# Performance work log

Measured on AMD Instinct MI355X. Metric: run time of the kernel, lower is better.

The kernel has to match this reference:

```python
import jax, jax.numpy as jnp
import numpy as np

# EfficientMemoryGEMMWithSoftmax forward: the returned value visible to the
# model is simply result = x1 @ x2 (batched GEMM of softmax probs with V).
# The outlier-statistics / sparse / SVD compression path only affects what is
# cached for the (lossy) backward; the forward output math is exact.

B, H, S, D = 2, 16, 2048, 64

def setup_inputs() -> dict:
    key = jax.random.key(0)
    k1, k2 = jax.random.split(key)
    # x1 ~ softmax probabilities: nonnegative, rows normalized over last axis
    logits = jax.random.normal(k1, (B, H, S, S), dtype=jnp.float32)
    x1 = jax.nn.softmax(logits, axis=-1)
    x2 = jax.random.normal(k2, (B, H, S, D), dtype=jnp.float32)
    return {"x1": x1, "x2": x2}

def reference(x1, x2):
    # [B,H,S,S] @ [B,H,S,D] -> [B,H,S,D]
    return jnp.einsum('bhsk,bhkd->bhsd', x1, x2)
```

## Files before the change

### kernel.cpp

```cpp
#include <hip/hip_runtime.h>
#include <hip/hip_bf16.h>


#define S_DIM 2048
#define D_DIM 64
#define BM 128
#define BK 128
#define NT (S_DIM / BK)
#define LDB (BK + 8)

typedef __attribute__((ext_vector_type(8))) short short8;
typedef __attribute__((ext_vector_type(4))) short short4v;
typedef __attribute__((ext_vector_type(4))) float f32x4;

__device__ __forceinline__ short f2bf(float x) {
    return __builtin_bit_cast(short, __float2bfloat16(x));
}

__global__ __launch_bounds__(512, 2)
void pv_gemm_kernel(const float* __restrict__ x1,
                    const float* __restrict__ x2,
                    float* __restrict__ out) {
    __shared__ short lds_b[2][D_DIM][LDB];

    int bid = blockIdx.x;
    int lb  = (bid & 7) * 64 + (bid >> 3);
    int bh   = lb >> 4;
    int mblk = lb & 15;
    int m0   = mblk * BM;

    int tid  = threadIdx.x;
    int lane = tid & 63;
    int w    = tid >> 6;

    int sd  = tid & 63;
    int skb = tid >> 6;
    const float* x2base = x2 + (size_t)bh * S_DIM * D_DIM + sd;

    int arow = m0 + w * 16 + (lane & 15);
    int kgrp = (lane >> 4) * 8;
    const float* abase = x1 + ((size_t)bh * S_DIM + arow) * S_DIM + kgrp;

    f32x4 acc[4];
#pragma unroll
    for (int i = 0; i < 4; ++i) acc[i] = (f32x4){0.f, 0.f, 0.f, 0.f};

    {
        float rs[16];
#pragma unroll
        for (int i = 0; i < 16; ++i)
            rs[i] = x2base[(size_t)(skb * 16 + i) * D_DIM];
#pragma unroll
        for (int j = 0; j < 4; ++j) {
            short4v v;
            v[0] = f2bf(rs[4 * j + 0]);
            v[1] = f2bf(rs[4 * j + 1]);
            v[2] = f2bf(rs[4 * j + 2]);
            v[3] = f2bf(rs[4 * j + 3]);
            *(short4v*)&lds_b[0][sd][skb * 16 + 4 * j] = v;
        }
    }

    int buf = 0;
    for (int t = 0; t < NT; ++t) {
        __syncthreads();

        float rn[16];
        if (t + 1 < NT) {
            const float* p = x2base + (size_t)(t + 1) * BK * D_DIM;
#pragma unroll
            for (int i = 0; i < 16; ++i)
                rn[i] = p[(size_t)(skb * 16 + i) * D_DIM];
        }

        const float* ab = abase + (size_t)t * BK;
#pragma unroll
        for (int kk = 0; kk < 4; ++kk) {
            float4 lo = *(const float4*)(ab + kk * 32);
            float4 hi = *(const float4*)(ab + kk * 32 + 4);
            short8 a;
            a[0] = f2bf(lo.x); a[1] = f2bf(lo.y); a[2] = f2bf(lo.z); a[3] = f2bf(lo.w);
            a[4] = f2bf(hi.x); a[5] = f2bf(hi.y); a[6] = f2bf(hi.z); a[7] = f2bf(hi.w);
#pragma unroll
            for (int ni = 0; ni < 4; ++ni) {
                int col = ni * 16 + (lane & 15);
                const short8* bp =
                    (const short8*)&lds_b[buf][col][kk * 32 + kgrp];
                acc[ni] = __builtin_amdgcn_mfma_f32_16x16x32_bf16(a, *bp, acc[ni], 0, 0, 0);
            }
        }

        if (t + 1 < NT) {
#pragma unroll
            for (int j = 0; j < 4; ++j) {
                short4v v;
                v[0] = f2bf(rn[4 * j + 0]);
                v[1] = f2bf(rn[4 * j + 1]);
                v[2] = f2bf(rn[4 * j + 2]);
                v[3] = f2bf(rn[4 * j + 3]);
                *(short4v*)&lds_b[buf ^ 1][sd][skb * 16 + 4 * j] = v;
            }
        }
        buf ^= 1;
    }

    int col0 = lane & 15;
    int r0   = m0 + w * 16 + ((lane >> 4) << 2);
    float* ob = out + ((size_t)bh * S_DIM + r0) * D_DIM + col0;
#pragma unroll
    for (int ni = 0; ni < 4; ++ni) {
#pragma unroll
        for (int r = 0; r < 4; ++r)
            ob[(size_t)r * D_DIM + ni * 16] = acc[ni][r];
    }
}

extern "C" void kernel_launch(void* const* d_in, const int* in_sizes, int n_in,
                              void* d_out, int out_size, void* d_ws, size_t ws_size,
                              hipStream_t stream) {
    const float* x1 = (const float*)d_in[0];
    const float* x2 = (const float*)d_in[1];
    float* out = (float*)d_out;

    dim3 grid(512);
    dim3 block(512);
    hipLaunchKernelGGL(pv_gemm_kernel, grid, block, 0, stream, x1, x2, out);
}
```

Before: 132.0 us.

## Prefetch A tiles into registers one step ahead and raise occupancy target

Loads the next K-tile of the fp32 probability matrix into a second register buffer while the current tile is converted and fed to MFMA. The loop is manually unrolled by two to alternate buffers. The launch bound is raised to request four blocks per CU. The aim is to hide global-load latency on the dominant x1 stream, at the cost of more live registers and a possible spill under the tighter register cap.

```diff
diff --git a/kernel.cpp b/kernel.cpp
--- a/kernel.cpp
+++ b/kernel.cpp
@@ -17,7 +17,7 @@
     return __builtin_bit_cast(short, __float2bfloat16(x));
 }
 
-__global__ __launch_bounds__(512, 2)
+__global__ __launch_bounds__(512, 4)
 void pv_gemm_kernel(const float* __restrict__ x1,
                     const float* __restrict__ x2,
                     float* __restrict__ out) {
@@ -61,48 +61,67 @@
         }
     }
 
-    int buf = 0;
-    for (int t = 0; t < NT; ++t) {
-        __syncthreads();
+    float4 rA0[8], rA1[8];
+#pragma unroll
+    for (int kk = 0; kk < 4; ++kk) {
+        rA0[2 * kk]     = *(const float4*)(abase + kk * 32);
+        rA0[2 * kk + 1] = *(const float4*)(abase + kk * 32 + 4);
+    }
 
-        float rn[16];
-        if (t + 1 < NT) {
-            const float* p = x2base + (size_t)(t + 1) * BK * D_DIM;
-#pragma unroll
-            for (int i = 0; i < 16; ++i)
-                rn[i] = p[(size_t)(skb * 16 + i) * D_DIM];
-        }
+#define ITER(T, RBUF, RA_CUR, RA_NXT)                                        \
+    {                                                                        \
+        __syncthreads();                                                     \
+        float rn[16];                                                        \
+        if ((T) + 1 < NT) {                                                  \
+                      \
+            const float* p = x2base + (size_t)((T) + 1) * BK * D_DIM;        \
+            _Pragma("unroll")                                                \
+            for (int i = 0; i < 16; ++i)                                     \
+                rn[i] = p[(size_t)(skb * 16 + i) * D_DIM];                   \
+            const float* an = abase + (size_t)((T) + 1) * BK;                \
+            _Pragma("unroll")                                                \
+            for (int kk = 0; kk < 4; ++kk) {                                 \
+                RA_NXT[2 * kk]     = *(const float4*)(an + kk * 32);         \
+                RA_NXT[2 * kk + 1] = *(const float4*)(an + kk * 32 + 4);     \
+            }                                                                \
+        }                                                                    \
+        _Pragma("unroll")                                                    \
+        for (int kk = 0; kk < 4; ++kk) {                                     \
+            short8 a;                                                        \
+            a[0] = f2bf(RA_CUR[2 * kk].x);                                   \
+            a[1] = f2bf(RA_CUR[2 * kk].y);                                   \
+            a[2] = f2bf(RA_CUR[2 * kk].z);                                   \
+            a[3] = f2bf(RA_CUR[2 * kk].w);                                   \
+            a[4] = f2bf(RA_CUR[2 * kk + 1].x);                               \
+            a[5] = f2bf(RA_CUR[2 * kk + 1].y);                               \
+            a[6] = f2bf(RA_CUR[2 * kk + 1].z);                               \
+            a[7] = f2bf(RA_CUR[2 * kk + 1].w);                               \
+            _Pragma("unroll")                                                \
+            for (int ni = 0; ni < 4; ++ni) {                                 \
+                const short8* bp = (const short8*)                           \
+                    &lds_b[RBUF][ni * 16 + (lane & 15)][kk * 32 + kgrp];     \
+                acc[ni] = __builtin_amdgcn_mfma_f32_16x16x32_bf16(           \
+                    a, *bp, acc[ni], 0, 0, 0);                               \
+            }                                                                \
+        }                                                                    \
+        if ((T) + 1 < NT) {                                                  \
+            _Pragma("unroll")                                                \
+            for (int j = 0; j < 4; ++j) {                                    \
+                short4v v;                                                   \
+                v[0] = f2bf(rn[4 * j + 0]);                                  \
+                v[1] = f2bf(rn[4 * j + 1]);                                  \
+                v[2] = f2bf(rn[4 * j + 2]);                                  \
+                v[3] = f2bf(rn[4 * j + 3]);                                  \
+                *(short4v*)&lds_b[(RBUF) ^ 1][sd][skb * 16 + 4 * j] = v;     \
+            }                                                                \
+        }                                                                    \
+    }
 
-        const float* ab = abase + (size_t)t * BK;
-#pragma unroll
-        for (int kk = 0; kk < 4; ++kk) {
-            float4 lo = *(const float4*)(ab + kk * 32);
-            float4 hi = *(const float4*)(ab + kk * 32 + 4);
-            short8 a;
-            a[0] = f2bf(lo.x); a[1] = f2bf(lo.y); a[2] = f2bf(lo.z); a[3] = f2bf(lo.w);
-            a[4] = f2bf(hi.x); a[5] = f2bf(hi.y); a[6] = f2bf(hi.z); a[7] = f2bf(hi.w);
-#pragma unroll
-            for (int ni = 0; ni < 4; ++ni) {
-                int col = ni * 16 + (lane & 15);
-                const short8* bp =
-                    (const short8*)&lds_b[buf][col][kk * 32 + kgrp];
-                acc[ni] = __builtin_amdgcn_mfma_f32_16x16x32_bf16(a, *bp, acc[ni], 0, 0, 0);
-            }
-        }
-
-        if (t + 1 < NT) {
-#pragma unroll
-            for (int j = 0; j < 4; ++j) {
-                short4v v;
-                v[0] = f2bf(rn[4 * j + 0]);
-                v[1] = f2bf(rn[4 * j + 1]);
-                v[2] = f2bf(rn[4 * j + 2]);
-                v[3] = f2bf(rn[4 * j + 3]);
-                *(short4v*)&lds_b[buf ^ 1][sd][skb * 16 + 4 * j] = v;
-            }
-        }
-        buf ^= 1;
+    for (int t = 0; t < NT; t += 2) {
+        ITER(t,     0, rA0, rA1);
+        ITER(t + 1, 1, rA1, rA0);
     }
+#undef ITER
 
     int col0 = lane & 15;
     int r0   = m0 + w * 16 + ((lane >> 4) << 2);
```

Result: faster. 116.8 us (-11.5%).

## Pre-transpose V to bf16 and read B operand directly from L2

Applied to the files above, without the earlier changes.

Adds a small pre-pass that converts x2 to bf16 and transposes it into workspace. The main GEMM then loads B fragments straight from global memory (L2-resident) instead of staging them through LDS, which removes the __syncthreads and LDS traffic. It also double-buffers the x1 loads in registers using nontemporal loads, and keeps the LDS kernel as a fallback when the workspace is too small. The cost is an extra kernel launch, extra register pressure, and more L2 traffic for B.

```diff
diff --git a/kernel.cpp b/kernel.cpp
--- a/kernel.cpp
+++ b/kernel.cpp
@@ -17,12 +17,36 @@
     return __builtin_bit_cast(short, __float2bfloat16(x));
 }
 
+__global__ __launch_bounds__(256)
+void x2_transpose_kernel(const float* __restrict__ x2, short* __restrict__ x2t) {
+    __shared__ float tile[64][65];
+    int bh = blockIdx.x >> 5;
+    int kb = (blockIdx.x & 31) * 64;
+    int t  = threadIdx.x;
+    int d  = t & 63;
+    int k4 = t >> 6;
+    const float* src = x2 + ((size_t)bh * S_DIM + kb) * D_DIM + d;
+#pragma unroll
+    for (int i = 0; i < 16; ++i)
+        tile[i * 4 + k4][d] = src[(size_t)(i * 4 + k4) * D_DIM];
+    __syncthreads();
+    int dcol = t >> 2;
+    int kg   = (t & 3) * 16;
+    short8 v0, v1;
+#pragma unroll
+    for (int j = 0; j < 8; ++j) {
+        v0[j] = f2bf(tile[kg + j][dcol]);
+        v1[j] = f2bf(tile[kg + 8 + j][dcol]);
+    }
+    short* dst = x2t + ((size_t)bh * D_DIM + dcol) * S_DIM + kb + kg;
+    *(short8*)dst = v0;
+    *(short8*)(dst + 8) = v1;
+}
+
 __global__ __launch_bounds__(512, 2)
-void pv_gemm_kernel(const float* __restrict__ x1,
-                    const float* __restrict__ x2,
-                    float* __restrict__ out) {
-    __shared__ short lds_b[2][D_DIM][LDB];
-
+void pv_gemm_l2b_kernel(const float* __restrict__ x1,
+                        const short* __restrict__ x2t,
+                        float* __restrict__ out) {
     int bid = blockIdx.x;
     int lb  = (bid & 7) * 64 + (bid >> 3);
     int bh   = lb >> 4;
@@ -33,18 +57,112 @@
     int lane = tid & 63;
     int w    = tid >> 6;
 
+    int arow = m0 + w * 16 + (lane & 15);
+    int kgrp = (lane >> 4) * 8;
+    const float* aptr = x1 + ((size_t)bh * S_DIM + arow) * S_DIM + kgrp;
+
+    const short* bbase = x2t + ((size_t)bh * D_DIM + (lane & 15)) * S_DIM + kgrp;
+    const short* bp_ni0 = bbase;
+    const short* bp_ni1 = bbase + (size_t)16 * S_DIM;
+    const short* bp_ni2 = bbase + (size_t)32 * S_DIM;
+    const short* bp_ni3 = bbase + (size_t)48 * S_DIM;
+
+    f32x4 acc[4];
+#pragma unroll
+    for (int i = 0; i < 4; ++i) acc[i] = (f32x4){0.f, 0.f, 0.f, 0.f};
+
+    f32x4 rA0[8], rA1[8];
+#pragma unroll
+    for (int kk = 0; kk < 4; ++kk) {
+        rA0[2 * kk]     = __builtin_nontemporal_load((const f32x4*)(aptr + kk * 32));
+        rA0[2 * kk + 1] = __builtin_nontemporal_load((const f32x4*)(aptr + kk * 32 + 4));
+    }
+
+#define ITER(T, RA_CUR, RA_NXT)                                               \
+    {                                                                         \
+        const short* b0 = bp_ni0 + (size_t)(T) * BK;                          \
+        const short* b1 = bp_ni1 + (size_t)(T) * BK;                          \
+        const short* b2 = bp_ni2 + (size_t)(T) * BK;                          \
+        const short* b3 = bp_ni3 + (size_t)(T) * BK;                          \
+        short8 vb[16];                                                        \
+        _Pragma("unroll")                                                     \
+        for (int kk = 0; kk < 4; ++kk) {                                      \
+            vb[kk * 4 + 0] = *(const short8*)(b0 + kk * 32);                  \
+            vb[kk * 4 + 1] = *(const short8*)(b1 + kk * 32);                  \
+            vb[kk * 4 + 2] = *(const short8*)(b2 + kk * 32);                  \
+            vb[kk * 4 + 3] = *(const short8*)(b3 + kk * 32);                  \
+        }                                                                     \
+        if ((T) + 1 < NT) {                                                   \
+            const float* an = aptr + (size_t)((T) + 1) * BK;                  \
+            _Pragma("unroll")                                                 \
+            for (int kk = 0; kk < 4; ++kk) {                                  \
+                RA_NXT[2 * kk] = __builtin_nontemporal_load(                  \
+                    (const f32x4*)(an + kk * 32));                            \
+                RA_NXT[2 * kk + 1] = __builtin_nontemporal_load(              \
+                    (const f32x4*)(an + kk * 32 + 4));                        \
+            }                                                                 \
+        }                                                                     \
+        _Pragma("unroll")                                                     \
+        for (int kk = 0; kk < 4; ++kk) {                                      \
+            short8 a;                                                         \
+            a[0] = f2bf(RA_CUR[2 * kk][0]);                                   \
+            a[1] = f2bf(RA_CUR[2 * kk][1]);                                   \
+            a[2] = f2bf(RA_CUR[2 * kk][2]);                                   \
+            a[3] = f2bf(RA_CUR[2 * kk][3]);                                   \
+            a[4] = f2bf(RA_CUR[2 * kk + 1][0]);                               \
+            a[5] = f2bf(RA_CUR[2 * kk + 1][1]);                               \
+            a[6] = f2bf(RA_CUR[2 * kk + 1][2]);                               \
+            a[7] = f2bf(RA_CUR[2 * kk + 1][3]);                               \
+            acc[0] = __builtin_amdgcn_mfma_f32_16x16x32_bf16(                 \
+                a, vb[kk * 4 + 0], acc[0], 0, 0, 0);                          \
+            acc[1] = __builtin_amdgcn_mfma_f32_16x16x32_bf16(                 \
+                a, vb[kk * 4 + 1], acc[1], 0, 0, 0);                          \
+            acc[2] = __builtin_amdgcn_mfma_f32_16x16x32_bf16(                 \
+                a, vb[kk * 4 + 2], acc[2], 0, 0, 0);                          \
+            acc[3] = __builtin_amdgcn_mfma_f32_16x16x32_bf16(                 \
+                a, vb[kk * 4 + 3], acc[3], 0, 0, 0);                          \
+        }                                                                     \
+    }
+
+    for (int t = 0; t < NT; t += 2) {
+        ITER(t,     rA0, rA1);
+        ITER(t + 1, rA1, rA0);
+    }
+#undef ITER
+
+    int col0 = lane & 15;
+    int r0   = m0 + w * 16 + ((lane >> 4) << 2);
+    float* ob = out + ((size_t)bh * S_DIM + r0) * D_DIM + col0;
+#pragma unroll
+    for (int ni = 0; ni < 4; ++ni) {
+#pragma unroll
+        for (int r = 0; r < 4; ++r)
+            ob[(size_t)r * D_DIM + ni * 16] = acc[ni][r];
+    }
+}
+
+__global__ __launch_bounds__(512, 4)
+void pv_gemm_lds_kernel(const float* __restrict__ x1,
+                        const float* __restrict__ x2,
+                        float* __restrict__ out) {
+    __shared__ short lds_b[2][D_DIM][LDB];
+    int bid = blockIdx.x;
+    int lb  = (bid & 7) * 64 + (bid >> 3);
+    int bh   = lb >> 4;
+    int mblk = lb & 15;
+    int m0   = mblk * BM;
+    int tid  = threadIdx.x;
+    int lane = tid & 63;
+    int w    = tid >> 6;
     int sd  = tid & 63;
     int skb = tid >> 6;
     const float* x2base = x2 + (size_t)bh * S_DIM * D_DIM + sd;
-
     int arow = m0 + w * 16 + (lane & 15);
     int kgrp = (lane >> 4) * 8;
     const float* abase = x1 + ((size_t)bh * S_DIM + arow) * S_DIM + kgrp;
-
     f32x4 acc[4];
 #pragma unroll
     for (int i = 0; i < 4; ++i) acc[i] = (f32x4){0.f, 0.f, 0.f, 0.f};
-
     {
         float rs[16];
 #pragma unroll
@@ -53,18 +171,14 @@
 #pragma unroll
         for (int j = 0; j < 4; ++j) {
             short4v v;
-            v[0] = f2bf(rs[4 * j + 0]);
-            v[1] = f2bf(rs[4 * j + 1]);
-            v[2] = f2bf(rs[4 * j + 2]);
-            v[3] = f2bf(rs[4 * j + 3]);
+            v[0] = f2bf(rs[4 * j + 0]); v[1] = f2bf(rs[4 * j + 1]);
+            v[2] = f2bf(rs[4 * j + 2]); v[3] = f2bf(rs[4 * j + 3]);
             *(short4v*)&lds_b[0][sd][skb * 16 + 4 * j] = v;
         }
     }
-
     int buf = 0;
     for (int t = 0; t < NT; ++t) {
         __syncthreads();
-
         float rn[16];
         if (t + 1 < NT) {
             const float* p = x2base + (size_t)(t + 1) * BK * D_DIM;
@@ -72,7 +186,6 @@
             for (int i = 0; i < 16; ++i)
                 rn[i] = p[(size_t)(skb * 16 + i) * D_DIM];
         }
-
         const float* ab = abase + (size_t)t * BK;
 #pragma unroll
         for (int kk = 0; kk < 4; ++kk) {
@@ -83,27 +196,22 @@
             a[4] = f2bf(hi.x); a[5] = f2bf(hi.y); a[6] = f2bf(hi.z); a[7] = f2bf(hi.w);
 #pragma unroll
             for (int ni = 0; ni < 4; ++ni) {
-                int col = ni * 16 + (lane & 15);
                 const short8* bp =
-                    (const short8*)&lds_b[buf][col][kk * 32 + kgrp];
+                    (const short8*)&lds_b[buf][ni * 16 + (lane & 15)][kk * 32 + kgrp];
                 acc[ni] = __builtin_amdgcn_mfma_f32_16x16x32_bf16(a, *bp, acc[ni], 0, 0, 0);
             }
         }
-
         if (t + 1 < NT) {
 #pragma unroll
             for (int j = 0; j < 4; ++j) {
                 short4v v;
-                v[0] = f2bf(rn[4 * j + 0]);
-                v[1] = f2bf(rn[4 * j + 1]);
-                v[2] = f2bf(rn[4 * j + 2]);
-                v[3] = f2bf(rn[4 * j + 3]);
+                v[0] = f2bf(rn[4 * j + 0]); v[1] = f2bf(rn[4 * j + 1]);
+                v[2] = f2bf(rn[4 * j + 2]); v[3] = f2bf(rn[4 * j + 3]);
                 *(short4v*)&lds_b[buf ^ 1][sd][skb * 16 + 4 * j] = v;
             }
         }
         buf ^= 1;
     }
-
     int col0 = lane & 15;
     int r0   = m0 + w * 16 + ((lane >> 4) << 2);
     float* ob = out + ((size_t)bh * S_DIM + r0) * D_DIM + col0;
@@ -122,7 +230,15 @@
     const float* x2 = (const float*)d_in[1];
     float* out = (float*)d_out;
 
-    dim3 grid(512);
-    dim3 block(512);
-    hipLaunchKernelGGL(pv_gemm_kernel, grid, block, 0, stream, x1, x2, out);
-}
+    const size_t need = (size_t)32 * D_DIM * S_DIM * sizeof(short);
+    if (ws_size >= need) {
+        short* x2t = (short*)d_ws;
+        hipLaunchKernelGGL(x2_transpose_kernel, dim3(1024), dim3(256), 0, stream,
+                           x2, x2t);
+        hipLaunchKernelGGL(pv_gemm_l2b_kernel, dim3(512), dim3(512), 0, stream,
+                           x1, x2t, out);
+    } else {
+        hipLaunchKernelGGL(pv_gemm_lds_kernel, dim3(512), dim3(512), 0, stream,
+                           x1, x2, out);
+    }
+}
```

Result: slower. 235.2 us (+78.2%).

## Split K in halves with whole-half B staged in LDS and atomic reduction

Applied to the files above, without the earlier changes.

Each block now covers a 256-row M tile and half of K. The whole 1024x64 bf16 slice of x2 is loaded into swizzled LDS once, which removes the per-step barriers and the double-buffered B. A-tile loads are register double-buffered, and each wave starts at a staggered K phase to spread DRAM and L2 traffic. Partial results are combined with float atomics into a zero-initialised output (an added memset), which costs extra atomic traffic and makes the summation order nondeterministic.

```diff
diff --git a/kernel.cpp b/kernel.cpp
--- a/kernel.cpp
+++ b/kernel.cpp
@@ -4,13 +4,12 @@
 
 #define S_DIM 2048
 #define D_DIM 64
-#define BM 128
-#define BK 128
-#define NT (S_DIM / BK)
-#define LDB (BK + 8)
+#define BM    256
+#define KH    1024
+#define BK    128
+#define NSTEP (KH / BK)
 
 typedef __attribute__((ext_vector_type(8))) short short8;
-typedef __attribute__((ext_vector_type(4))) short short4v;
 typedef __attribute__((ext_vector_type(4))) float f32x4;
 
 __device__ __forceinline__ short f2bf(float x) {
@@ -18,100 +17,136 @@
 }
 
 __global__ __launch_bounds__(512, 2)
-void pv_gemm_kernel(const float* __restrict__ x1,
+void pv_gemm_splitk(const float* __restrict__ x1,
                     const float* __restrict__ x2,
                     float* __restrict__ out) {
-    __shared__ short lds_b[2][D_DIM][LDB];
+    __shared__ short ldsB[D_DIM * KH];
 
     int bid = blockIdx.x;
     int lb  = (bid & 7) * 64 + (bid >> 3);
     int bh   = lb >> 4;
-    int mblk = lb & 15;
+    int mblk = (lb >> 1) & 7;
+    int kh   = lb & 1;
     int m0   = mblk * BM;
+    int k0   = kh * KH;
 
     int tid  = threadIdx.x;
     int lane = tid & 63;
     int w    = tid >> 6;
 
-    int sd  = tid & 63;
-    int skb = tid >> 6;
-    const float* x2base = x2 + (size_t)bh * S_DIM * D_DIM + sd;
+    int ll = lane & 15;
+    int lh = lane >> 4;
+    int xr = lane & 7;
 
-    int arow = m0 + w * 16 + (lane & 15);
-    int kgrp = (lane >> 4) * 8;
-    const float* abase = x1 + ((size_t)bh * S_DIM + arow) * S_DIM + kgrp;
+    const float* aw = x1 + ((size_t)bh * S_DIM + m0 + w * 16 + ll) * S_DIM + k0 + lh * 8;
 
-    f32x4 acc[4];
+    int phase = (w + mblk + (kh << 2)) & 7;
+
+    f32x4 rA0[16], rA1[16];
+    {
+        const float* an = aw + (size_t)phase * BK;
 #pragma unroll
-    for (int i = 0; i < 4; ++i) acc[i] = (f32x4){0.f, 0.f, 0.f, 0.f};
-
-    {
-        float rs[16];
+        for (int mr = 0; mr < 2; ++mr) {
+            const float* am = an + (size_t)mr * 128 * S_DIM;
 #pragma unroll
-        for (int i = 0; i < 16; ++i)
-            rs[i] = x2base[(size_t)(skb * 16 + i) * D_DIM];
-#pragma unroll
-        for (int j = 0; j < 4; ++j) {
-            short4v v;
-            v[0] = f2bf(rs[4 * j + 0]);
-            v[1] = f2bf(rs[4 * j + 1]);
-            v[2] = f2bf(rs[4 * j + 2]);
-            v[3] = f2bf(rs[4 * j + 3]);
-            *(short4v*)&lds_b[0][sd][skb * 16 + 4 * j] = v;
+            for (int kk = 0; kk < 4; ++kk) {
+                rA0[mr * 8 + 2 * kk]     = *(const f32x4*)(am + kk * 32);
+                rA0[mr * 8 + 2 * kk + 1] = *(const f32x4*)(am + kk * 32 + 4);
+            }
         }
     }
 
-    int buf = 0;
-    for (int t = 0; t < NT; ++t) {
-        __syncthreads();
+    {
+        const float* xb = x2 + ((size_t)bh * S_DIM + k0) * D_DIM + lane;
+        char* lrow = (char*)ldsB + (size_t)lane * (KH * 2);
+        int dxr = lane & 7;
+#pragma unroll
+        for (int it = 0; it < 16; ++it) {
+            int ko = w * 16 + it;
+            const float* p = xb + (size_t)ko * 8 * D_DIM;
+            short8 v;
+#pragma unroll
+            for (int i = 0; i < 8; ++i)
+                v[i] = f2bf(p[(size_t)i * D_DIM]);
+            *(short8*)(lrow + ((ko ^ dxr) << 4)) = v;
+        }
+    }
+    __syncthreads();
 
-        float rn[16];
-        if (t + 1 < NT) {
-            const float* p = x2base + (size_t)(t + 1) * BK * D_DIM;
+    f32x4 acc[8];
 #pragma unroll
-            for (int i = 0; i < 16; ++i)
-                rn[i] = p[(size_t)(skb * 16 + i) * D_DIM];
-        }
+    for (int i = 0; i < 8; ++i) acc[i] = (f32x4){0.f, 0.f, 0.f, 0.f};
 
-        const float* ab = abase + (size_t)t * BK;
+    char* b0r = (char*)ldsB + (size_t)(0 * 16 + ll) * (KH * 2);
+    char* b1r = (char*)ldsB + (size_t)(1 * 16 + ll) * (KH * 2);
+    char* b2r = (char*)ldsB + (size_t)(2 * 16 + ll) * (KH * 2);
+    char* b3r = (char*)ldsB + (size_t)(3 * 16 + ll) * (KH * 2);
+
+#define STEP(S, RA_CUR, RA_NXT)                                               \
+    {                                                                         \
+        if ((S) + 1 < NSTEP) {                                                \
+            int kn = ((S) + 1 + phase) & 7;                                   \
+            const float* an = aw + (size_t)kn * BK;                           \
+            _Pragma("unroll")                                                 \
+            for (int mr = 0; mr < 2; ++mr) {                                  \
+                const float* am = an + (size_t)mr * 128 * S_DIM;              \
+                _Pragma("unroll")                                             \
+                for (int kk = 0; kk < 4; ++kk) {                              \
+                    RA_NXT[mr * 8 + 2 * kk]     = *(const f32x4*)(am + kk * 32);      \
+                    RA_NXT[mr * 8 + 2 * kk + 1] = *(const f32x4*)(am + kk * 32 + 4);  \
+                }                                                             \
+            }                                                                 \
+        }                                                                     \
+        int kob = (((S) + phase) & 7) * 16;                                   \
+        _Pragma("unroll")                                                     \
+        for (int kk = 0; kk < 4; ++kk) {                                      \
+            int koq = ((kob + kk * 4 + lh) ^ xr) << 4;                        \
+            short8 vb0 = *(const short8*)(b0r + koq);                         \
+            short8 vb1 = *(const short8*)(b1r + koq);                         \
+            short8 vb2 = *(const short8*)(b2r + koq);                         \
+            short8 vb3 = *(const short8*)(b3r + koq);                         \
+            _Pragma("unroll")                                                 \
+            for (int mr = 0; mr < 2; ++mr) {                                  \
+                short8 a;                                                     \
+                a[0] = f2bf(RA_CUR[mr * 8 + 2 * kk][0]);                      \
+                a[1] = f2bf(RA_CUR[mr * 8 + 2 * kk][1]);                      \
+                a[2] = f2bf(RA_CUR[mr * 8 + 2 * kk][2]);                      \
+                a[3] = f2bf(RA_CUR[mr * 8 + 2 * kk][3]);                      \
+                a[4] = f2bf(RA_CUR[mr * 8 + 2 * kk + 1][0]);                  \
+                a[5] = f2bf(RA_CUR[mr * 8 + 2 * kk + 1][1]);                  \
+                a[6] = f2bf(RA_CUR[mr * 8 + 2 * kk + 1][2]);                  \
+                a[7] = f2bf(RA_CUR[mr * 8 + 2 * kk + 1][3]);                  \
+                acc[mr * 4 + 0] = __builtin_amdgcn_mfma_f32_16x16x32_bf16(    \
+                    a, vb0, acc[mr * 4 + 0], 0, 0, 0);                        \
+                acc[mr * 4 + 1] = __builtin_amdgcn_mfma_f32_16x16x32_bf16(    \
+                    a, vb1, acc[mr * 4 + 1], 0, 0, 0);                        \
+                acc[mr * 4 + 2] = __builtin_amdgcn_mfma_f32_16x16x32_bf16(    \
+                    a, vb2, acc[mr * 4 + 2], 0, 0, 0);                        \
+                acc[mr * 4 + 3] = __builtin_amdgcn_mfma_f32_16x16x32_bf16(    \
+                    a, vb3, acc[mr * 4 + 3], 0, 0, 0);                        \
+            }                                                                 \
+        }                                                                     \
+    }
+
+    for (int s = 0; s < NSTEP; s += 2) {
+        STEP(s,     rA0, rA1);
+        STEP(s + 1, rA1, rA0);
+    }
+#undef STEP
+
+    int r0 = m0 + w * 16 + lh * 4;
 #pragma unroll
-        for (int kk = 0; kk < 4; ++kk) {
-            float4 lo = *(const float4*)(ab + kk * 32);
-            float4 hi = *(const float4*)(ab + kk * 32 + 4);
-            short8 a;
-            a[0] = f2bf(lo.x); a[1] = f2bf(lo.y); a[2] = f2bf(lo.z); a[3] = f2bf(lo.w);
-            a[4] = f2bf(hi.x); a[5] = f2bf(hi.y); a[6] = f2bf(hi.z); a[7] = f2bf(hi.w);
+    for (int mr = 0; mr < 2; ++mr) {
 #pragma unroll
-            for (int ni = 0; ni < 4; ++ni) {
-                int col = ni * 16 + (lane & 15);
-                const short8* bp =
-                    (const short8*)&lds_b[buf][col][kk * 32 + kgrp];
-                acc[ni] = __builtin_amdgcn_mfma_f32_16x16x32_bf16(a, *bp, acc[ni], 0, 0, 0);
+        for (int ni = 0; ni < 4; ++ni) {
+#pragma unroll
+            for (int r = 0; r < 4; ++r) {
+                float* p = out + ((size_t)bh * S_DIM + r0 + mr * 128 + r) * D_DIM
+                             + ni * 16 + ll;
+                __hip_atomic_fetch_add(p, acc[mr * 4 + ni][r],
+                                       __ATOMIC_RELAXED, __HIP_MEMORY_SCOPE_AGENT);
             }
         }
-
-        if (t + 1 < NT) {
-#pragma unroll
-            for (int j = 0; j < 4; ++j) {
-                short4v v;
-                v[0] = f2bf(rn[4 * j + 0]);
-                v[1] = f2bf(rn[4 * j + 1]);
-                v[2] = f2bf(rn[4 * j + 2]);
-                v[3] = f2bf(rn[4 * j + 3]);
-                *(short4v*)&lds_b[buf ^ 1][sd][skb * 16 + 4 * j] = v;
-            }
-        }
-        buf ^= 1;
-    }
-
-    int col0 = lane & 15;
-    int r0   = m0 + w * 16 + ((lane >> 4) << 2);
-    float* ob = out + ((size_t)bh * S_DIM + r0) * D_DIM + col0;
-#pragma unroll
-    for (int ni = 0; ni < 4; ++ni) {
-#pragma unroll
-        for (int r = 0; r < 4; ++r)
-            ob[(size_t)r * D_DIM + ni * 16] = acc[ni][r];
     }
 }
 
@@ -122,7 +157,7 @@
     const float* x2 = (const float*)d_in[1];
     float* out = (float*)d_out;
 
-    dim3 grid(512);
-    dim3 block(512);
-    hipLaunchKernelGGL(pv_gemm_kernel, grid, block, 0, stream, x1, x2, out);
+    hipMemsetAsync(d_out, 0, (size_t)out_size * sizeof(float), stream);
+    hipLaunchKernelGGL(pv_gemm_splitk, dim3(512), dim3(512), 0, stream,
+                       x1, x2, out);
 }
```

After: 137.1 us. 3.9% more time.
